# Optimization experiments

Hardware: AMD Instinct MI355X
Metric: run time of the kernel (lower is better)

## Reference

```python
import jax, jax.numpy as jnp
import numpy as np

BATCH, SEQ, EMBED = 8, 1024, 2048
HEADS, LATENT = 16, 512
HEAD_DIM = EMBED // HEADS            # 128
NOPE = HEAD_DIM // 4                 # 32 (qk_rope_dim=96 is even, no adjust)
ROPE_D = HEAD_DIM - NOPE             # 96
THETA = 10000.0


def _rope_tables(seq_len):
    # matches torch: freqs over arange(0, rope_dim, 2)/rope_dim
    freqs = 1.0 / THETA ** (jnp.arange(0, ROPE_D, 2, dtype=jnp.float32) / ROPE_D)
    emb = jnp.arange(seq_len, dtype=jnp.float32)[:, None] * freqs[None, :]  # [S, ROPE_D//2]
    return jnp.cos(emb), jnp.sin(emb)


def _apply_rope(x, cos, sin):
    # x: [B,H,S,D]; cos/sin: [S,D//2]. NOTE: original concatenates halves (non-interleaved output).
    xe, xo = x[..., ::2], x[..., 1::2]
    return jnp.concatenate([xe * cos - xo * sin, xo * cos + xe * sin], axis=-1)


def setup_inputs() -> dict:
    key = jax.random.key(0)
    ks = jax.random.split(key, 5)
    x = jax.random.normal(ks[0], (BATCH, SEQ, EMBED), jnp.float32)
    Wq = jax.random.normal(ks[1], (EMBED, EMBED), jnp.float32) * 0.02
    Wkv_down = jax.random.normal(ks[2], (EMBED, LATENT), jnp.float32) * 0.02
    Wk_up = jax.random.normal(ks[3], (LATENT, EMBED), jnp.float32) * 0.02
    Wv_up = jax.random.normal(ks[4], (LATENT, EMBED), jnp.float32) * 0.02
    return {"x": x, "Wq": Wq, "Wkv_down": Wkv_down, "Wk_up": Wk_up, "Wv_up": Wv_up}


def reference(x, Wq, Wkv_down, Wk_up, Wv_up):
    B, S, E = x.shape
    # projections (weights stored [in, out], equivalent to nn.Linear math)
    q = (x @ Wq).reshape(B, S, HEADS, HEAD_DIM).transpose(0, 2, 1, 3)   # [B,H,S,D]
    q_nope, q_rope = q[..., :NOPE], q[..., NOPE:]
    c_kv = x @ Wkv_down                                                  # [B,S,latent]
    k = (c_kv @ Wk_up).reshape(B, S, HEADS, HEAD_DIM).transpose(0, 2, 1, 3)
    v = (c_kv @ Wv_up).reshape(B, S, HEADS, HEAD_DIM).transpose(0, 2, 1, 3)
    k_nope, k_rope = k[..., :NOPE], k[..., NOPE:]

    cos, sin = _rope_tables(S)
    q_rope = _apply_rope(q_rope, cos, sin)
    k_rope = _apply_rope(k_rope, cos, sin)

    qf = jnp.concatenate([q_nope, q_rope], axis=-1)
    kf = jnp.concatenate([k_nope, k_rope], axis=-1)

    scale = jnp.float32(1.0 / np.sqrt(HEAD_DIM))
    scores = jnp.einsum('bhqd,bhkd->bhqk', qf, kf) * scale
    causal = jnp.triu(jnp.ones((S, S), dtype=bool), k=1)  # past_length=0
    scores = jnp.where(causal, -jnp.inf, scores)
    weights = jax.nn.softmax(scores, axis=-1)
    out = jnp.einsum('bhqk,bhkd->bhqd', weights, v)
    return out.transpose(0, 2, 1, 3).reshape(B, S, E)
```

## Files before the change

### kernel.cpp

```cpp
#include <hip/hip_runtime.h>
#include <stdint.h>

typedef unsigned short u16;
typedef __bf16 bf16x8 __attribute__((ext_vector_type(8)));
typedef float    f32x4 __attribute__((ext_vector_type(4)));
typedef unsigned short u16x8 __attribute__((ext_vector_type(8)));
typedef unsigned short u16x4 __attribute__((ext_vector_type(4)));

#define BB 8
#define SS 1024
#define EE 2048
#define HH 16
#define DD 128

__device__ __forceinline__ u16 f2bf(float f){
  union { float f; unsigned u; } v; v.f = f;
  unsigned r = v.u + 0x7FFFu + ((v.u >> 16) & 1u);
  return (u16)(r >> 16);
}
__device__ __forceinline__ float bf2f(u16 h){
  union { unsigned u; float f; } v; v.u = ((unsigned)h) << 16;
  return v.f;
}
__device__ __forceinline__ bf16x8 ld8(const u16* p){
  return __builtin_bit_cast(bf16x8, *(const u16x8*)p);
}

typedef __attribute__((address_space(1))) const unsigned int gas_u32;
typedef __attribute__((address_space(3))) unsigned int las_u32;
__device__ __forceinline__ void g2l16(const u16* g, u16* l){
  __builtin_amdgcn_global_load_lds((gas_u32*)g, (las_u32*)l, 16, 0, 0);
}

#define BARRIER() asm volatile("s_barrier" ::: "memory")
#define VMC(n)    asm volatile("s_waitcnt vmcnt(" #n ")" ::: "memory")

__device__ __forceinline__ void trB(const float* __restrict__ W, u16* __restrict__ Wt,
                                    int K, int N, int bx, int by,
                                    float (*t)[33], int tid){
  int c = tid & 31, r = tid >> 5;
  #pragma unroll
  for (int i = 0; i < 32; i += 8)
    t[r+i][c] = W[(size_t)(by*32 + r + i)*N + bx*32 + c];
  __syncthreads();
  #pragma unroll
  for (int i = 0; i < 32; i += 8)
    Wt[(size_t)(bx*32 + r + i)*K + by*32 + c] = f2bf(t[c][r+i]);
}

__global__ __launch_bounds__(256) void prep(const float* __restrict__ x, u16* __restrict__ xb,
    const float* __restrict__ Wq,   u16* __restrict__ WqT,
    const float* __restrict__ Wkvd, u16* __restrict__ WkvdT,
    const float* __restrict__ Wku,  u16* __restrict__ WkuT,
    const float* __restrict__ Wvu,  u16* __restrict__ WvuT,
    float* __restrict__ cosb, float* __restrict__ sinb){
  __shared__ float t[32][33];
  const int bid = blockIdx.x, tid = threadIdx.x;
  if (bid < 8192){
    int i = (bid*256 + tid)*8;
    float4 v0 = *(const float4*)(x + i);
    float4 v1 = *(const float4*)(x + i + 4);
    u16x8 o;
    o[0]=f2bf(v0.x); o[1]=f2bf(v0.y); o[2]=f2bf(v0.z); o[3]=f2bf(v0.w);
    o[4]=f2bf(v1.x); o[5]=f2bf(v1.y); o[6]=f2bf(v1.z); o[7]=f2bf(v1.w);
    *(u16x8*)(xb + i) = o;
  } else if (bid < 12288){
    int k = bid - 8192;  trB(Wq,   WqT,   EE,  EE,  k & 63, k >> 6, t, tid);
  } else if (bid < 13312){
    int k = bid - 12288; trB(Wkvd, WkvdT, EE,  512, k & 15, k >> 4, t, tid);
  } else if (bid < 14336){
    int k = bid - 13312; trB(Wku,  WkuT,  512, EE,  k & 63, k >> 6, t, tid);
  } else if (bid < 15360){
    int k = bid - 14336; trB(Wvu,  WvuT,  512, EE,  k & 63, k >> 6, t, tid);
  } else {
    int i = (bid - 15360)*256 + tid;
    if (i < SS*48){
      int s = i / 48, j = i % 48;
      float freq = powf(10000.0f, -((float)(2*j)) / 96.0f);
      float e = (float)s * freq;
      cosb[i] = cosf(e);
      sinb[i] = sinf(e);
    }
  }
}

__global__ __launch_bounds__(256) void rope_apply2(u16* __restrict__ qp,
                                                   u16* __restrict__ kp,
                                                   const float* __restrict__ cosb,
                                                   const float* __restrict__ sinb){
  u16* base = blockIdx.y ? kp : qp;
  int t = blockIdx.x*256 + threadIdx.x;
  int row = t >> 4, h = t & 15, s = row & (SS-1);
  u16* p = base + (size_t)row*EE + h*DD + 32;
  float e[48], o[48];
  #pragma unroll
  for (int c = 0; c < 12; c++){
    u16x8 v = *(const u16x8*)(p + c*8);
    #pragma unroll
    for (int j = 0; j < 4; j++){
      e[c*4 + j] = bf2f(v[2*j]);
      o[c*4 + j] = bf2f(v[2*j+1]);
    }
  }
  u16 ob[96];
  #pragma unroll
  for (int j = 0; j < 48; j++){
    float cs = cosb[s*48 + j], sn = sinb[s*48 + j];
    ob[j]      = f2bf(e[j]*cs - o[j]*sn);
    ob[48 + j] = f2bf(o[j]*cs + e[j]*sn);
  }
  #pragma unroll
  for (int c = 0; c < 12; c++)
    *(u16x8*)(p + c*8) = *(const u16x8*)(ob + c*8);
}

__global__ __launch_bounds__(256) void gemm_bt(const u16* __restrict__ A,
    const u16* __restrict__ Bt, u16* __restrict__ C, int M, int N, int K){
  __shared__ u16 Al[128*32];
  __shared__ u16 Bl[128*32];
  const int tid = threadIdx.x;
  const int lane = tid & 63, w = tid >> 6;
  const int wr = w >> 1, wc = w & 1;
  const int l15 = lane & 15, l4 = lane >> 4;
  const int id = blockIdx.y * 4 + blockIdx.x;
  const int xcd = id & 7, j = id >> 3;
  const int bm = (xcd*8 + (j >> 2)) * 128;
  const int bn = (j & 3) * 128;
  const int srow = tid >> 2;
  const int skc  = (tid & 3) * 8;
  const u16* ga = A  + (size_t)(bm + srow)*K + skc;
  const u16* gb = Bt + (size_t)(bn + srow)*K + skc;
  u16* la = Al + w*512;
  u16* lb = Bl + w*512;
  f32x4 acc[4][4] = {};
  for (int k0 = 0; k0 < K; k0 += 32){
    __syncthreads();
    g2l16(ga + k0,          la);
    g2l16(ga + 64*K + k0,   la + 2048);
    g2l16(gb + k0,          lb);
    g2l16(gb + 64*K + k0,   lb + 2048);
    __syncthreads();
    bf16x8 af[4], bfr[4];
    #pragma unroll
    for (int m = 0; m < 4; m++) af[m]  = ld8(Al + (wr*64 + m*16 + l15)*32 + l4*8);
    #pragma unroll
    for (int n = 0; n < 4; n++) bfr[n] = ld8(Bl + (wc*64 + n*16 + l15)*32 + l4*8);
    #pragma unroll
    for (int m = 0; m < 4; m++)
      #pragma unroll
      for (int n = 0; n < 4; n++)
        acc[m][n] = __builtin_amdgcn_mfma_f32_16x16x32_bf16(af[m], bfr[n], acc[m][n], 0, 0, 0);
  }
  #pragma unroll
  for (int m = 0; m < 4; m++)
    #pragma unroll
    for (int n = 0; n < 4; n++)
      #pragma unroll
      for (int r = 0; r < 4; r++){
        int row = bm + wr*64 + m*16 + l4*4 + r;
        int col = bn + wc*64 + n*16 + l15;
        C[(size_t)row*N + col] = f2bf(acc[m][n][r]);
      }
}

#define AFR(ab, mf, ks) ld8(&AL[ab][wr][((mf)*16 + l15)*64 + ((((ks)*4 + l4) ^ r7) << 3)])
#define BFR(bb, nf, ks) ld8(&BL[bb][wc>>1][(((wc&1)*64 + (nf)*16 + l15))*64 + ((((ks)*4 + l4) ^ r7) << 3)])

#define STAGE_A(ab, h, kt) stage2(aRow, (h), (kt), K, &AL[ab][h][0], wj0)
#define STAGE_A2(ab, kt)   do{ STAGE_A(ab, 0, kt); STAGE_A(ab, 1, kt); }while(0)
#define STAGE_B(bb, h, kt) stage2(bRow, (h), (kt), K, &BL[bb][h][0], wj0)

__device__ __forceinline__ void stage2(const u16* rowbase, int h, int kt, int K,
                                       u16* lds, int wj0){
  const u16* g = rowbase + (size_t)h*128*K + kt*64;
  g2l16(g,               lds + wj0*512);
  g2l16(g + (size_t)8*K, lds + wj0*512 + 512);
}

#define PHASE(ab, q, LOADB, STAGE, DOVM) do{                                       \
  bf16x8 a00 = AFR(ab, 2*(q)  , 0);                                               \
  bf16x8 a01 = AFR(ab, 2*(q)  , 1);                                               \
  bf16x8 a10 = AFR(ab, 2*(q)+1, 0);                                               \
  bf16x8 a11 = AFR(ab, 2*(q)+1, 1);                                               \
  if (LOADB){                                                                      \
    _Pragma("unroll")                                                              \
    for (int nf = 0; nf < 4; nf++){ bq[nf][0]=BFR(ab,nf,0); bq[nf][1]=BFR(ab,nf,1); } \
  }                                                                                \
  STAGE;                                                                           \
  if (DOVM) VMC(4);                                                                \
  BARRIER();                                                                       \
  __builtin_amdgcn_s_setprio(1);                                                   \
  _Pragma("unroll")                                                                \
  for (int nf = 0; nf < 4; nf++){                                                  \
    acc[2*(q)][nf]   = __builtin_amdgcn_mfma_f32_16x16x32_bf16(a00, bq[nf][0], acc[2*(q)][nf],0,0,0);   \
    acc[2*(q)+1][nf] = __builtin_amdgcn_mfma_f32_16x16x32_bf16(a10, bq[nf][0], acc[2*(q)+1][nf],0,0,0); \
  }                                                                                \
  _Pragma("unroll")                                                                \
  for (int nf = 0; nf < 4; nf++){                                                  \
    acc[2*(q)][nf]   = __builtin_amdgcn_mfma_f32_16x16x32_bf16(a01, bq[nf][1], acc[2*(q)][nf],0,0,0);   \
    acc[2*(q)+1][nf] = __builtin_amdgcn_mfma_f32_16x16x32_bf16(a11, bq[nf][1], acc[2*(q)+1][nf],0,0,0); \
  }                                                                                \
  __builtin_amdgcn_s_setprio(0);                                                   \
  BARRIER();                                                                       \
  __builtin_amdgcn_sched_barrier(0);                                               \
}while(0)

__global__ __launch_bounds__(512, 2) void gemm8(const u16* __restrict__ A,
    const u16* __restrict__ Bt, u16* __restrict__ C0, u16* __restrict__ C1,
    int K, int Nout0, int Nout1, int nsplit, int vt){
  __shared__ u16 AL[2][2][128*64];
  __shared__ u16 BL[2][2][128*64];
  const int tid = threadIdx.x, lane = tid & 63, w = tid >> 6;
  const int wr = w >> 2, wc = w & 3;
  const int l15 = lane & 15, l4 = lane >> 4;
  const int r7 = l15 & 7;
  const int nbx = gridDim.x;
  const int lb  = __popc(nbx - 1);
  const int id  = blockIdx.y * nbx + blockIdx.x;
  const int xcd = id & 7, j = id >> 3;
  const int rpx = gridDim.y >> 3;
  const int bm  = (xcd*rpx + (j >> lb)) * 256;
  const int bn  = (j & (nbx - 1)) * 256;
  const int wj0 = w*2;
  const int cswz = (lane & 7) ^ (lane >> 3);
  const u16* aRow = A  + (size_t)(bm + wj0*8 + (lane>>3))*K + cswz*8;
  const u16* bRow = Bt + (size_t)(bn + wj0*8 + (lane>>3))*K + cswz*8;

  const int nkt = K >> 6;
  const int niter = nkt >> 1;

  STAGE_A2(0, 0);
  STAGE_B(0, 0, 0); STAGE_B(0, 1, 0);
  STAGE_B(1, 0, 1); STAGE_B(1, 1, 1);
  VMC(4);
  BARRIER();

  f32x4 acc[8][4] = {};
  bf16x8 bq[4][2];

  for (int it = 0; it < niter; ++it){
    const int kt1 = 2*it + 1;
    int kt2 = 2*it + 2; if (kt2 >= nkt) kt2 -= nkt;
    int kt3 = 2*it + 3; if (kt3 >= nkt) kt3 -= nkt;
    PHASE(0, 0, 1, STAGE_A2(1, kt1),    0);
    PHASE(0, 1, 0, STAGE_B(0, 0, kt2),  0);
    PHASE(0, 2, 0, STAGE_B(0, 1, kt2),  0);
    PHASE(0, 3, 0, ;,                   1);
    PHASE(1, 0, 1, STAGE_A2(0, kt2),    0);
    PHASE(1, 1, 0, STAGE_B(1, 0, kt3),  0);
    PHASE(1, 2, 0, STAGE_B(1, 1, kt3),  0);
    PHASE(1, 3, 0, ;,                   1);
  }
  asm volatile("s_waitcnt vmcnt(0)" ::: "memory");

  if (vt && bn >= nsplit){
    const int bcol = bn - nsplit;
    #pragma unroll
    for (int mf = 0; mf < 8; mf++)
      #pragma unroll
      for (int nf = 0; nf < 4; nf++){
        int row0 = bm + wr*128 + mf*16 + l4*4;
        int col  = bcol + wc*64 + nf*16 + l15;
        int bh = (row0 >> 10)*16 + (col >> 7);
        int d  = col & 127;
        int s  = row0 & 1023;
        u16x4 pk;
        #pragma unroll
        for (int r = 0; r < 4; r++) pk[r] = f2bf(acc[mf][nf][r]);
        *(u16x4*)(C1 + (((size_t)(bh*128 + d)) << 10) + s) = pk;
      }
  } else {
    u16* Cd = (bn < nsplit) ? C0 : C1;
    const int No = (bn < nsplit) ? Nout0 : Nout1;
    const int bcol = (bn < nsplit) ? bn : bn - nsplit;
    #pragma unroll
    for (int mf = 0; mf < 8; mf++)
      #pragma unroll
      for (int nf = 0; nf < 4; nf++)
        #pragma unroll
        for (int r = 0; r < 4; r++){
          int row = bm + wr*128 + mf*16 + l4*4 + r;
          int col = bcol + wc*64 + nf*16 + l15;
          Cd[(size_t)row*No + col] = f2bf(acc[mf][nf][r]);
        }
  }
}

#define PLW 40

__global__ __launch_bounds__(512) void attn(const u16* __restrict__ qp,
                                            const u16* __restrict__ kp,
                                            const u16* __restrict__ vpT,
                                            float* __restrict__ out){
  __shared__ u16 Kl[2][64*128];
  __shared__ u16 Vl[2][128*64];
  __shared__ u16 Pl[8][16*PLW];
  const int tid = threadIdx.x, lane = tid & 63, w = tid >> 6;
  const int l15 = lane & 15, l4 = lane >> 4;
  const int qt = 7 - blockIdx.y;
  const int bh = blockIdx.x;
  const int b = bh >> 4, h = bh & 15;
  const int qbase = qt*128;
  const int qmin = qbase + w*16;
  const int qg = qmin + l15;
  const float c = 0.12751920700948998f;
  const float THR = 62.7f;

  const size_t rowq = (size_t)(b*SS + qg)*EE + h*DD;
  bf16x8 qf[4];
  #pragma unroll
  for (int kk = 0; kk < 4; kk++) qf[kk] = ld8(qp + rowq + kk*32 + l4*8);
  #pragma unroll
  for (int kk = 0; kk < 4; kk++) asm volatile("" : "+v"(qf[kk]));

  f32x4 ao[8] = {};
  float mi = -3e38f, li = 0.0f;

  const int ntiles = 2*qt + 2;
  const int vcc = lane & 7;

  #pragma unroll
  for (int q = 0; q < 2; q++){
    int r = w*8 + q*4 + (lane>>4);
    g2l16(kp + (size_t)(b*SS + r)*EE + h*DD + (((lane&15) ^ (r&7))<<3),
          &Kl[0][0] + w*1024 + q*512);
    int d = w*16 + q*8 + (lane>>3);
    g2l16(vpT + (size_t)(bh*DD + d)*SS + ((vcc ^ (d&7))<<3),
          &Vl[0][0] + w*1024 + q*512);
  }

  for (int t = 0; t < ntiles; t++){
    const int kv0 = t*64;
    const int buf = t & 1;
    {
      const int kvn = (t + 1 < ntiles) ? kv0 + 64 : kv0;
      #pragma unroll
      for (int q = 0; q < 2; q++){
        int r = w*8 + q*4 + (lane>>4);
        g2l16(kp + (size_t)(b*SS + kvn + r)*EE + h*DD + (((lane&15) ^ (r&7))<<3),
              &Kl[buf^1][0] + w*1024 + q*512);
        int d = w*16 + q*8 + (lane>>3);
        g2l16(vpT + (size_t)(bh*DD + d)*SS + kvn + ((vcc ^ (d&7))<<3),
              &Vl[buf^1][0] + w*1024 + q*512);
      }
    }
    VMC(4);
    BARRIER();

    if (kv0 <= qmin + 15){
      float sv[4][4];
      __builtin_amdgcn_s_setprio(1);
      #pragma unroll
      for (int nt = 0; nt < 4; nt++){
        f32x4 sacc = {};
        #pragma unroll
        for (int kk = 0; kk < 4; kk++){
          bf16x8 kf = ld8(&Kl[buf][0] + (nt*16 + l15)*128 + (((kk*4 + l4) ^ (l15&7))<<3));
          sacc = __builtin_amdgcn_mfma_f32_16x16x32_bf16(kf, qf[kk], sacc, 0, 0, 0);
        }
        #pragma unroll
        for (int r = 0; r < 4; r++) sv[nt][r] = sacc[r];
      }
      __builtin_amdgcn_s_setprio(0);
      if (kv0 + 63 > qmin){
        #pragma unroll
        for (int nt = 0; nt < 4; nt++)
          #pragma unroll
          for (int r = 0; r < 4; r++){
            int kg = kv0 + nt*16 + l4*4 + r;
            if (kg > qg) sv[nt][r] = -3e38f;
          }
      }
      float mx = sv[0][0];
      #pragma unroll
      for (int nt = 0; nt < 4; nt++)
        #pragma unroll
        for (int r = 0; r < 4; r++) mx = fmaxf(mx, sv[nt][r]);
      mx = fmaxf(mx, __shfl_xor(mx, 16));
      mx = fmaxf(mx, __shfl_xor(mx, 32));
      if (__any(mx > mi + THR)){
        float mnew = fmaxf(mi, mx);
        float alpha = __builtin_amdgcn_exp2f((mi - mnew)*c);
        li *= alpha;
        #pragma unroll
        for (int n8 = 0; n8 < 8; n8++) ao[n8] *= alpha;
        mi = mnew;
      }
      const float mnc = mi*c;
      float pout[4][4];
      float rs = 0.0f;
      #pragma unroll
      for (int nt = 0; nt < 4; nt++)
        #pragma unroll
        for (int r = 0; r < 4; r++){
          float pv = __builtin_amdgcn_exp2f(__builtin_fmaf(sv[nt][r], c, -mnc));
          pout[nt][r] = pv; rs += pv;
        }
      rs += __shfl_xor(rs, 16);
      rs += __shfl_xor(rs, 32);
      li += rs;
      #pragma unroll
      for (int kk = 0; kk < 2; kk++){
        #pragma unroll
        for (int ntl = 0; ntl < 2; ntl++){
          int nt = kk*2 + ntl;
          u16x4 pk;
          #pragma unroll
          for (int r = 0; r < 4; r++) pk[r] = f2bf(pout[nt][r]);
          *(u16x4*)(&Pl[w][l15*PLW + ntl*16 + l4*4]) = pk;
        }
        bf16x8 pa = ld8(&Pl[w][l15*PLW + l4*8]);
        __builtin_amdgcn_s_setprio(1);
        #pragma unroll
        for (int n8 = 0; n8 < 8; n8++){
          bf16x8 vf = ld8(&Vl[buf][0] + (n8*16 + l15)*64 + (((kk*4 + l4) ^ (l15&7))<<3));
          ao[n8] = __builtin_amdgcn_mfma_f32_16x16x32_bf16(vf, pa, ao[n8], 0, 0, 0);
        }
        __builtin_amdgcn_s_setprio(0);
      }
    }
    BARRIER();
  }
  asm volatile("s_waitcnt vmcnt(0)" ::: "memory");

  const float inv = 1.0f / li;
  const size_t orow = (size_t)(b*SS + qg)*EE + h*DD;
  #pragma unroll
  for (int n8 = 0; n8 < 8; n8++){
    f32x4 o = ao[n8]*inv;
    *(float4*)(out + orow + n8*16 + l4*4) = __builtin_bit_cast(float4, o);
  }
}

extern "C" void kernel_launch(void* const* d_in, const int* in_sizes, int n_in,
                              void* d_out, int out_size, void* d_ws, size_t ws_size,
                              hipStream_t stream){
  const float* x    = (const float*)d_in[0];
  const float* Wq   = (const float*)d_in[1];
  const float* Wkvd = (const float*)d_in[2];
  const float* Wku  = (const float*)d_in[3];
  const float* Wvu  = (const float*)d_in[4];
  float* out = (float*)d_out;
  char* ws = (char*)d_ws;

  u16*   xb    = (u16*)  (ws);
  u16*   WqT   = (u16*)  (ws +  33554432);
  u16*   WkvdT = (u16*)  (ws +  41943040);
  u16*   WkuT  = (u16*)  (ws +  44040192);
  u16*   WvuT  = (u16*)  (ws +  46137344);
  float* cosb  = (float*)(ws +  48234496);
  float* sinb  = (float*)(ws +  48431104);
  u16*   qp    = (u16*)  (ws +  48627712);
  u16*   ckv   = (u16*)  (ws +  82182144);
  u16*   kp    = (u16*)  (ws +  90570752);
  u16*   vpT   = (u16*)  (ws + 124125184);

  prep<<<15552, 256, 0, stream>>>(x, xb, Wq, WqT, Wkvd, WkvdT,
                                  Wku, WkuT, Wvu, WvuT, cosb, sinb);

  gemm8<<<dim3(EE/256, (BB*SS)/256), 512, 0, stream>>>(xb, WqT, qp, qp,
                                                       EE, EE, EE, EE, 0);
  gemm_bt<<<dim3(512/128, (BB*SS)/128), 256, 0, stream>>>(xb, WkvdT, ckv, BB*SS, 512, EE);
  gemm8<<<dim3(4096/256, (BB*SS)/256), 512, 0, stream>>>(ckv, WkuT, kp, vpT,
                                                         512, EE, 0, EE, 1);

  rope_apply2<<<dim3((BB*SS*HH)/256, 2), 256, 0, stream>>>(qp, kp, cosb, sinb);

  attn<<<dim3(BB*HH, SS/128), 512, 0, stream>>>(qp, kp, vpT, out);
}
```

Measured before the change: 286.4 us.

## Restructure gemm8 to 256x128 tiles with B fragments loaded directly to registers

The projection GEMM tile shrinks from 256x256 to 256x128 and the B operand is no longer staged through LDS. Each wave now loads its B fragments straight from global memory into double-buffered registers, while A stays LDS-staged. Launch bounds rise to four blocks per CU, and block-to-XCD mapping now spreads the N dimension across XCDs. The aim is to halve LDS use, remove B LDS traffic and raise occupancy, at the cost of less reuse per tile, more global reads of B, and a full vmcnt(0) wait every tile.

```diff
diff --git a/kernel.cpp b/kernel.cpp
--- a/kernel.cpp
+++ b/kernel.cpp
@@ -163,12 +163,10 @@
       }
 }
 
-#define AFR(ab, mf, ks) ld8(&AL[ab][wr][((mf)*16 + l15)*64 + ((((ks)*4 + l4) ^ r7) << 3)])
-#define BFR(bb, nf, ks) ld8(&BL[bb][wc>>1][(((wc&1)*64 + (nf)*16 + l15))*64 + ((((ks)*4 + l4) ^ r7) << 3)])
+#define AFR(ab, mf, ks) ld8(&AL[ab][wr>>1][(((wr&1)*64 + (mf)*16 + l15))*64 + ((((ks)*4 + l4) ^ r7) << 3)])
 
 #define STAGE_A(ab, h, kt) stage2(aRow, (h), (kt), K, &AL[ab][h][0], wj0)
 #define STAGE_A2(ab, kt)   do{ STAGE_A(ab, 0, kt); STAGE_A(ab, 1, kt); }while(0)
-#define STAGE_B(bb, h, kt) stage2(bRow, (h), (kt), K, &BL[bb][h][0], wj0)
 
 __device__ __forceinline__ void stage2(const u16* rowbase, int h, int kt, int K,
                                        u16* lds, int wj0){
@@ -177,89 +175,79 @@
   g2l16(g + (size_t)8*K, lds + wj0*512 + 512);
 }
 
-#define PHASE(ab, q, LOADB, STAGE, DOVM) do{                                       \
-  bf16x8 a00 = AFR(ab, 2*(q)  , 0);                                               \
-  bf16x8 a01 = AFR(ab, 2*(q)  , 1);                                               \
-  bf16x8 a10 = AFR(ab, 2*(q)+1, 0);                                               \
-  bf16x8 a11 = AFR(ab, 2*(q)+1, 1);                                               \
-  if (LOADB){                                                                      \
-    _Pragma("unroll")                                                              \
-    for (int nf = 0; nf < 4; nf++){ bq[nf][0]=BFR(ab,nf,0); bq[nf][1]=BFR(ab,nf,1); } \
+#define LOADB(dst, kt) do{                                                         \
+  _Pragma("unroll")                                                                \
+  for (int nf = 0; nf < 4; nf++){                                                  \
+    dst[nf][0] = ld8(bW + (size_t)(nf*16)*K + (kt)*64);                            \
+    dst[nf][1] = ld8(bW + (size_t)(nf*16)*K + (kt)*64 + 32);                       \
   }                                                                                \
-  STAGE;                                                                           \
-  if (DOVM) VMC(4);                                                                \
-  BARRIER();                                                                       \
+}while(0)
+
+#define TILE(ab, BQ, BQN, ktn) do{                                                 \
+  STAGE_A2((ab)^1, ktn);                                                           \
+  LOADB(BQN, ktn);                                                                 \
+  __builtin_amdgcn_sched_barrier(0);                                               \
   __builtin_amdgcn_s_setprio(1);                                                   \
   _Pragma("unroll")                                                                \
-  for (int nf = 0; nf < 4; nf++){                                                  \
-    acc[2*(q)][nf]   = __builtin_amdgcn_mfma_f32_16x16x32_bf16(a00, bq[nf][0], acc[2*(q)][nf],0,0,0);   \
-    acc[2*(q)+1][nf] = __builtin_amdgcn_mfma_f32_16x16x32_bf16(a10, bq[nf][0], acc[2*(q)+1][nf],0,0,0); \
-  }                                                                                \
-  _Pragma("unroll")                                                                \
-  for (int nf = 0; nf < 4; nf++){                                                  \
-    acc[2*(q)][nf]   = __builtin_amdgcn_mfma_f32_16x16x32_bf16(a01, bq[nf][1], acc[2*(q)][nf],0,0,0);   \
-    acc[2*(q)+1][nf] = __builtin_amdgcn_mfma_f32_16x16x32_bf16(a11, bq[nf][1], acc[2*(q)+1][nf],0,0,0); \
-  }                                                                                \
+  for (int ks = 0; ks < 2; ks++)                                                   \
+    _Pragma("unroll")                                                              \
+    for (int mf = 0; mf < 4; mf++){                                                \
+      bf16x8 af = AFR(ab, mf, ks);                                                 \
+      _Pragma("unroll")                                                            \
+      for (int nf = 0; nf < 4; nf++)                                               \
+        acc[mf][nf] = __builtin_amdgcn_mfma_f32_16x16x32_bf16(af, BQ[nf][ks], acc[mf][nf], 0, 0, 0); \
+    }                                                                              \
   __builtin_amdgcn_s_setprio(0);                                                   \
+  VMC(0);                                                                          \
   BARRIER();                                                                       \
-  __builtin_amdgcn_sched_barrier(0);                                               \
 }while(0)
 
-__global__ __launch_bounds__(512, 2) void gemm8(const u16* __restrict__ A,
+__global__ __launch_bounds__(512, 4) void gemm8(const u16* __restrict__ A,
     const u16* __restrict__ Bt, u16* __restrict__ C0, u16* __restrict__ C1,
     int K, int Nout0, int Nout1, int nsplit, int vt){
   __shared__ u16 AL[2][2][128*64];
-  __shared__ u16 BL[2][2][128*64];
   const int tid = threadIdx.x, lane = tid & 63, w = tid >> 6;
-  const int wr = w >> 2, wc = w & 3;
+  const int wr = w >> 1, wc = w & 1;
   const int l15 = lane & 15, l4 = lane >> 4;
   const int r7 = l15 & 7;
   const int nbx = gridDim.x;
-  const int lb  = __popc(nbx - 1);
+  const int bnp = nbx >> 3;
+  const int lbn = __popc(bnp - 1);
   const int id  = blockIdx.y * nbx + blockIdx.x;
   const int xcd = id & 7, j = id >> 3;
-  const int rpx = gridDim.y >> 3;
-  const int bm  = (xcd*rpx + (j >> lb)) * 256;
-  const int bn  = (j & (nbx - 1)) * 256;
+  const int bn  = (xcd*bnp + (j & (bnp - 1))) * 128;
+  const int bm  = (j >> lbn) * 256;
   const int wj0 = w*2;
   const int cswz = (lane & 7) ^ (lane >> 3);
   const u16* aRow = A  + (size_t)(bm + wj0*8 + (lane>>3))*K + cswz*8;
-  const u16* bRow = Bt + (size_t)(bn + wj0*8 + (lane>>3))*K + cswz*8;
+  const u16* bW   = Bt + (size_t)(bn + wc*64 + l15)*K + l4*8;
 
   const int nkt = K >> 6;
   const int niter = nkt >> 1;
 
+  f32x4 acc[4][4] = {};
+  bf16x8 bqA[4][2], bqB[4][2];
+
   STAGE_A2(0, 0);
-  STAGE_B(0, 0, 0); STAGE_B(0, 1, 0);
-  STAGE_B(1, 0, 1); STAGE_B(1, 1, 1);
-  VMC(4);
+  LOADB(bqA, 0);
+  VMC(0);
   BARRIER();
-
-  f32x4 acc[8][4] = {};
-  bf16x8 bq[4][2];
 
   for (int it = 0; it < niter; ++it){
     const int kt1 = 2*it + 1;
     int kt2 = 2*it + 2; if (kt2 >= nkt) kt2 -= nkt;
-    int kt3 = 2*it + 3; if (kt3 >= nkt) kt3 -= nkt;
-    PHASE(0, 0, 1, STAGE_A2(1, kt1),    0);
-    PHASE(0, 1, 0, STAGE_B(0, 0, kt2),  0);
-    PHASE(0, 2, 0, STAGE_B(0, 1, kt2),  0);
-    PHASE(0, 3, 0, ;,                   1);
-    PHASE(1, 0, 1, STAGE_A2(0, kt2),    0);
-    PHASE(1, 1, 0, STAGE_B(1, 0, kt3),  0);
-    PHASE(1, 2, 0, STAGE_B(1, 1, kt3),  0);
-    PHASE(1, 3, 0, ;,                   1);
+    TILE(0, bqA, bqB, kt1);
+    TILE(1, bqB, bqA, kt2);
   }
   asm volatile("s_waitcnt vmcnt(0)" ::: "memory");
 
   if (vt && bn >= nsplit){
     const int bcol = bn - nsplit;
     #pragma unroll
-    for (int mf = 0; mf < 8; mf++)
+    for (int mf = 0; mf < 4; mf++)
       #pragma unroll
       for (int nf = 0; nf < 4; nf++){
-        int row0 = bm + wr*128 + mf*16 + l4*4;
+        int row0 = bm + wr*64 + mf*16 + l4*4;
         int col  = bcol + wc*64 + nf*16 + l15;
         int bh = (row0 >> 10)*16 + (col >> 7);
         int d  = col & 127;
@@ -274,12 +262,12 @@
     const int No = (bn < nsplit) ? Nout0 : Nout1;
     const int bcol = (bn < nsplit) ? bn : bn - nsplit;
     #pragma unroll
-    for (int mf = 0; mf < 8; mf++)
+    for (int mf = 0; mf < 4; mf++)
       #pragma unroll
       for (int nf = 0; nf < 4; nf++)
         #pragma unroll
         for (int r = 0; r < 4; r++){
-          int row = bm + wr*128 + mf*16 + l4*4 + r;
+          int row = bm + wr*64 + mf*16 + l4*4 + r;
           int col = bcol + wc*64 + nf*16 + l15;
           Cd[(size_t)row*No + col] = f2bf(acc[mf][nf][r]);
         }
@@ -458,10 +446,10 @@
   prep<<<15552, 256, 0, stream>>>(x, xb, Wq, WqT, Wkvd, WkvdT,
                                   Wku, WkuT, Wvu, WvuT, cosb, sinb);
 
-  gemm8<<<dim3(EE/256, (BB*SS)/256), 512, 0, stream>>>(xb, WqT, qp, qp,
+  gemm8<<<dim3(EE/128, (BB*SS)/256), 512, 0, stream>>>(xb, WqT, qp, qp,
                                                        EE, EE, EE, EE, 0);
   gemm_bt<<<dim3(512/128, (BB*SS)/128), 256, 0, stream>>>(xb, WkvdT, ckv, BB*SS, 512, EE);
-  gemm8<<<dim3(4096/256, (BB*SS)/256), 512, 0, stream>>>(ckv, WkuT, kp, vpT,
+  gemm8<<<dim3(4096/128, (BB*SS)/256), 512, 0, stream>>>(ckv, WkuT, kp, vpT,
                                                          512, EE, 0, EE, 1);
 
   rope_apply2<<<dim3((BB*SS*HH)/256, 2), 256, 0, stream>>>(qp, kp, cosb, sinb);
```

Result: slower. 492.3 us (+71.9%).

## Fuse Q projection and KV down-projection into one gemm8 launch

Applied to the files above, without the earlier changes.

Removes the separate small gemm_bt kernel that computed c_kv and extends the gemm8 grid from 2048 to 2560 output columns, so Q and the latent c_kv come from one launch that reads x once. Column blocks past nsplit write to the ckv buffer with their own output stride. Block index mapping changes from shift/mask to div/mod to support the non-power-of-two column-block count. This relies on WqT and WkvdT being contiguous in the workspace (they are, at adjacent offsets) so the B operand spans both weights.

```diff
diff --git a/kernel.cpp b/kernel.cpp
--- a/kernel.cpp
+++ b/kernel.cpp
@@ -114,55 +114,6 @@
     *(u16x8*)(p + c*8) = *(const u16x8*)(ob + c*8);
 }
 
-__global__ __launch_bounds__(256) void gemm_bt(const u16* __restrict__ A,
-    const u16* __restrict__ Bt, u16* __restrict__ C, int M, int N, int K){
-  __shared__ u16 Al[128*32];
-  __shared__ u16 Bl[128*32];
-  const int tid = threadIdx.x;
-  const int lane = tid & 63, w = tid >> 6;
-  const int wr = w >> 1, wc = w & 1;
-  const int l15 = lane & 15, l4 = lane >> 4;
-  const int id = blockIdx.y * 4 + blockIdx.x;
-  const int xcd = id & 7, j = id >> 3;
-  const int bm = (xcd*8 + (j >> 2)) * 128;
-  const int bn = (j & 3) * 128;
-  const int srow = tid >> 2;
-  const int skc  = (tid & 3) * 8;
-  const u16* ga = A  + (size_t)(bm + srow)*K + skc;
-  const u16* gb = Bt + (size_t)(bn + srow)*K + skc;
-  u16* la = Al + w*512;
-  u16* lb = Bl + w*512;
-  f32x4 acc[4][4] = {};
-  for (int k0 = 0; k0 < K; k0 += 32){
-    __syncthreads();
-    g2l16(ga + k0,          la);
-    g2l16(ga + 64*K + k0,   la + 2048);
-    g2l16(gb + k0,          lb);
-    g2l16(gb + 64*K + k0,   lb + 2048);
-    __syncthreads();
-    bf16x8 af[4], bfr[4];
-    #pragma unroll
-    for (int m = 0; m < 4; m++) af[m]  = ld8(Al + (wr*64 + m*16 + l15)*32 + l4*8);
-    #pragma unroll
-    for (int n = 0; n < 4; n++) bfr[n] = ld8(Bl + (wc*64 + n*16 + l15)*32 + l4*8);
-    #pragma unroll
-    for (int m = 0; m < 4; m++)
-      #pragma unroll
-      for (int n = 0; n < 4; n++)
-        acc[m][n] = __builtin_amdgcn_mfma_f32_16x16x32_bf16(af[m], bfr[n], acc[m][n], 0, 0, 0);
-  }
-  #pragma unroll
-  for (int m = 0; m < 4; m++)
-    #pragma unroll
-    for (int n = 0; n < 4; n++)
-      #pragma unroll
-      for (int r = 0; r < 4; r++){
-        int row = bm + wr*64 + m*16 + l4*4 + r;
-        int col = bn + wc*64 + n*16 + l15;
-        C[(size_t)row*N + col] = f2bf(acc[m][n][r]);
-      }
-}
-
 #define AFR(ab, mf, ks) ld8(&AL[ab][wr][((mf)*16 + l15)*64 + ((((ks)*4 + l4) ^ r7) << 3)])
 #define BFR(bb, nf, ks) ld8(&BL[bb][wc>>1][(((wc&1)*64 + (nf)*16 + l15))*64 + ((((ks)*4 + l4) ^ r7) << 3)])
 
@@ -215,12 +166,11 @@
   const int l15 = lane & 15, l4 = lane >> 4;
   const int r7 = l15 & 7;
   const int nbx = gridDim.x;
-  const int lb  = __popc(nbx - 1);
   const int id  = blockIdx.y * nbx + blockIdx.x;
   const int xcd = id & 7, j = id >> 3;
   const int rpx = gridDim.y >> 3;
-  const int bm  = (xcd*rpx + (j >> lb)) * 256;
-  const int bn  = (j & (nbx - 1)) * 256;
+  const int bn  = (j % nbx) * 256;
+  const int bm  = (xcd*rpx + (j / nbx)) * 256;
   const int wj0 = w*2;
   const int cswz = (lane & 7) ^ (lane >> 3);
   const u16* aRow = A  + (size_t)(bm + wj0*8 + (lane>>3))*K + cswz*8;
@@ -458,9 +408,8 @@
   prep<<<15552, 256, 0, stream>>>(x, xb, Wq, WqT, Wkvd, WkvdT,
                                   Wku, WkuT, Wvu, WvuT, cosb, sinb);
 
-  gemm8<<<dim3(EE/256, (BB*SS)/256), 512, 0, stream>>>(xb, WqT, qp, qp,
-                                                       EE, EE, EE, EE, 0);
-  gemm_bt<<<dim3(512/128, (BB*SS)/128), 256, 0, stream>>>(xb, WkvdT, ckv, BB*SS, 512, EE);
+  gemm8<<<dim3(2560/256, (BB*SS)/256), 512, 0, stream>>>(xb, WqT, qp, ckv,
+                                                         EE, EE, 512, EE, 0);
   gemm8<<<dim3(4096/256, (BB*SS)/256), 512, 0, stream>>>(ckv, WkuT, kp, vpT,
                                                          512, EE, 0, EE, 1);
 
```

Measured after the change: 287.9 us. About the same (+0.5%).
